# Optimization experiments

Measured on AMD Instinct MI355X. Metric: run time of the kernel, lower is better.

The kernel has to match this reference:

```python
import jax, jax.numpy as jnp
import numpy as np

N_NODES = 40000
N_EDGES = 640000
IN_CH = 128
OUT_CH = 128
BN_EPS = 1e-5


def setup_inputs() -> dict:
    key = jax.random.key(0)
    ks = jax.random.split(key, 8)
    x = jax.random.normal(ks[0], (N_NODES, IN_CH), dtype=jnp.float32)
    edge_index = jax.random.randint(ks[1], (2, N_EDGES), 0, N_NODES, dtype=jnp.int64)
    s1 = 1.0 / np.sqrt(IN_CH)
    s2 = 1.0 / np.sqrt(OUT_CH)
    W1 = jax.random.uniform(ks[2], (OUT_CH, IN_CH), jnp.float32, -s1, s1)
    b1 = jax.random.uniform(ks[3], (OUT_CH,), jnp.float32, -s1, s1)
    gamma = jnp.ones((OUT_CH,), jnp.float32)
    beta = jnp.zeros((OUT_CH,), jnp.float32)
    W2 = jax.random.uniform(ks[4], (OUT_CH, OUT_CH), jnp.float32, -s2, s2)
    b2 = jax.random.uniform(ks[5], (OUT_CH,), jnp.float32, -s2, s2)
    eps = jnp.float32(0.0)
    return {"x": x, "edge_index": edge_index, "W1": W1, "b1": b1,
            "gamma": gamma, "beta": beta, "W2": W2, "b2": b2, "eps": eps}


def reference(x, edge_index, W1, b1, gamma, beta, W2, b2, eps):
    src, dst = edge_index[0], edge_index[1]
    # neighbor sum: agg[v] = sum_{(u,v) in E} x[u]
    agg = jax.ops.segment_sum(x[src], dst, num_segments=N_NODES)  # [N, in_ch]
    h = (1.0 + eps) * x + agg
    # Linear 1
    h = h @ W1.T + b1  # [N, out_ch]
    # BatchNorm1d (training mode: batch stats, biased variance)
    mu = jnp.mean(h, axis=0)
    var = jnp.var(h, axis=0)
    h = (h - mu) * jax.lax.rsqrt(var + BN_EPS) * gamma + beta
    # ReLU + Linear 2
    h = jnp.maximum(h, 0.0)
    return h @ W2.T + b2
```

## Files before the change

### kernel.cpp

```cpp
#include <hip/hip_runtime.h>

#define NN 40000
#define NE 640000
#define BN_EPS 1e-5f

typedef __attribute__((ext_vector_type(8))) short bf16x8;
typedef __attribute__((ext_vector_type(4))) float f32x4;
typedef unsigned int uint;
typedef unsigned short ushort;

__device__ __forceinline__ float blo(uint u) { return __uint_as_float(u << 16); }
__device__ __forceinline__ float bhi(uint u) { return __uint_as_float(u & 0xFFFF0000u); }
__device__ __forceinline__ uint bpack(float lo, float hi) {
    uint a = __float_as_uint(lo); a = (a + 0x7FFFu + ((a >> 16) & 1u)) >> 16;
    uint b = __float_as_uint(hi); b = (b + 0x7FFFu + ((b >> 16) & 1u)) & 0xFFFF0000u;
    return a | b;
}
__device__ __forceinline__ ushort b1pack(float v) {
    uint u = __float_as_uint(v); return (ushort)((u + 0x7FFFu + ((u >> 16) & 1u)) >> 16);
}
__device__ __forceinline__ uint4 cvt8(const float4* f4, int i) {
    float4 p = f4[i * 2], q = f4[i * 2 + 1];
    uint4 o;
    o.x = bpack(p.x, p.y); o.y = bpack(p.z, p.w);
    o.z = bpack(q.x, q.y); o.w = bpack(q.z, q.w);
    return o;
}

__global__ __launch_bounds__(256) void k_pre(const float* __restrict__ x, const float* __restrict__ W1,
                                             const float* __restrict__ W2,
                                             int* __restrict__ cnt, float* __restrict__ bn,
                                             uint* __restrict__ xb, uint* __restrict__ w1b,
                                             uint* __restrict__ w2b) {
    int b = blockIdx.x, t = threadIdx.x;
    if (b < 157) {
        int i = b * 256 + t;
        if (i < NN) cnt[i] = 0;
        if (b == 156) bn[t] = 0.f;
    } else if (b < 2657) {
        int i = (b - 157) * 256 + t;
        ((uint4*)xb)[i] = cvt8((const float4*)x, i);
    } else if (b < 2665) {
        int i = (b - 2657) * 256 + t;
        ((uint4*)w1b)[i] = cvt8((const float4*)W1, i);
    } else {
        int i = (b - 2665) * 256 + t;
        ((uint4*)w2b)[i] = cvt8((const float4*)W2, i);
    }
}

__global__ __launch_bounds__(256) void k_bucket(const int* __restrict__ ei, int* __restrict__ cnt,
                                                ushort* __restrict__ srcl) {
    int e = blockIdx.x * 256 + threadIdx.x;
    if (e >= NE) return;
    int s = ei[e];
    int d = ei[NE + e];
    int pos = atomicAdd(&cnt[d], 1);
    if (pos < 64) srcl[d * 64 + pos] = (ushort)s;
}

__global__ __launch_bounds__(256) void k_gather(const uint* __restrict__ xbv, const int* __restrict__ cnt,
                                                const ushort* __restrict__ srcl, const float* __restrict__ epsp,
                                                uint* __restrict__ hb) {
    int wid = blockIdx.x * 4 + (threadIdx.x >> 6);
    int lane = threadIdx.x & 63;
    int deg = cnt[wid]; deg = deg > 64 ? 64 : deg;
    int sv = srcl[wid * 64 + lane];
    uint su = xbv[wid * 64 + lane];
    float e1 = 1.f + epsp[0];
    float a0 = blo(su) * e1, a1 = bhi(su) * e1;
    float c0 = 0.f, c1 = 0.f;
    int full = deg & ~7;
    for (int i = 0; i < full; i += 8) {
        int s0 = __builtin_amdgcn_readlane(sv, i);
        int s1 = __builtin_amdgcn_readlane(sv, i + 1);
        int s2 = __builtin_amdgcn_readlane(sv, i + 2);
        int s3 = __builtin_amdgcn_readlane(sv, i + 3);
        int s4 = __builtin_amdgcn_readlane(sv, i + 4);
        int s5 = __builtin_amdgcn_readlane(sv, i + 5);
        int s6 = __builtin_amdgcn_readlane(sv, i + 6);
        int s7 = __builtin_amdgcn_readlane(sv, i + 7);
        uint v0 = xbv[(size_t)s0 * 64 + lane];
        uint v1 = xbv[(size_t)s1 * 64 + lane];
        uint v2 = xbv[(size_t)s2 * 64 + lane];
        uint v3 = xbv[(size_t)s3 * 64 + lane];
        uint v4 = xbv[(size_t)s4 * 64 + lane];
        uint v5 = xbv[(size_t)s5 * 64 + lane];
        uint v6 = xbv[(size_t)s6 * 64 + lane];
        uint v7 = xbv[(size_t)s7 * 64 + lane];
        a0 += blo(v0) + blo(v1) + blo(v2) + blo(v3);
        c0 += blo(v4) + blo(v5) + blo(v6) + blo(v7);
        a1 += bhi(v0) + bhi(v1) + bhi(v2) + bhi(v3);
        c1 += bhi(v4) + bhi(v5) + bhi(v6) + bhi(v7);
    }
    if (deg & 7) {
#pragma unroll
        for (int j = 0; j < 8; ++j) {
            int idx = full + j;
            int s = __builtin_amdgcn_readlane(sv, idx);
            bool ok = idx < deg;
            s = ok ? s : 0;
            uint v = xbv[(size_t)s * 64 + lane];
            a0 += ok ? blo(v) : 0.f;
            a1 += ok ? bhi(v) : 0.f;
        }
    }
    hb[wid * 64 + lane] = bpack(a0 + c0, a1 + c1);
}

__global__ __launch_bounds__(256) void k_mm1(const ushort* __restrict__ hb, const ushort* __restrict__ w1b,
                                             const float* __restrict__ b1, ushort* __restrict__ h1b,
                                             float* __restrict__ bnsum, float* __restrict__ bnsumsq) {
    __shared__ float rs[256 * 8];
    __shared__ float rq[256 * 8];
    const int tid = threadIdx.x;
    const int wave = tid >> 6;
    const int lane = tid & 63;
    const int lr = lane & 15;
    const int lk = lane >> 4;
    const int r0 = (blockIdx.x * 4 + wave) * 16;

    bf16x8 a[4];
#pragma unroll
    for (int ks = 0; ks < 4; ++ks)
        a[ks] = *reinterpret_cast<const bf16x8*>(&hb[(size_t)(r0 + lr) * 128 + ks * 32 + lk * 8]);

    f32x4 acc[8];
#pragma unroll
    for (int t = 0; t < 8; ++t) { acc[t][0] = 0.f; acc[t][1] = 0.f; acc[t][2] = 0.f; acc[t][3] = 0.f; }

#pragma unroll
    for (int t = 0; t < 8; ++t) {
        const ushort* wrow = &w1b[(size_t)(t * 16 + lr) * 128];
#pragma unroll
        for (int ks = 0; ks < 4; ++ks) {
            bf16x8 bfr = *reinterpret_cast<const bf16x8*>(&wrow[ks * 32 + lk * 8]);
            acc[t] = __builtin_amdgcn_mfma_f32_16x16x32_bf16(a[ks], bfr, acc[t], 0, 0, 0);
        }
    }
#pragma unroll
    for (int t = 0; t < 8; ++t) {
        float bias = b1[t * 16 + lr];
        float s = 0.f, q = 0.f;
#pragma unroll
        for (int i = 0; i < 4; ++i) {
            float v = acc[t][i] + bias;
            h1b[(size_t)(r0 + lk * 4 + i) * 128 + t * 16 + lr] = b1pack(v);
            s += v; q += v * v;
        }
        rs[tid * 8 + t] = s;
        rq[tid * 8 + t] = q;
    }
    __syncthreads();
    if (tid < 128) {
        int c = tid, t = c >> 4, cr = c & 15;
        float s = 0.f, q = 0.f;
#pragma unroll
        for (int w = 0; w < 4; ++w)
#pragma unroll
            for (int g = 0; g < 4; ++g) {
                int src = w * 64 + g * 16 + cr;
                s += rs[src * 8 + t];
                q += rq[src * 8 + t];
            }
        atomicAdd(&bnsum[c], s);
        atomicAdd(&bnsumsq[c], q);
    }
}

__global__ __launch_bounds__(256) void k_mm2(const ushort* __restrict__ h1b, const ushort* __restrict__ w2b,
                                             const float* __restrict__ b2,
                                             const float* __restrict__ bnsum, const float* __restrict__ bnsumsq,
                                             const float* __restrict__ gamma, const float* __restrict__ beta,
                                             float* __restrict__ out) {
    __shared__ float ssc[128], ssh[128];
    const int tid = threadIdx.x;
    if (tid < 128) {
        float mu = bnsum[tid] * (1.0f / NN);
        float var = bnsumsq[tid] * (1.0f / NN) - mu * mu;
        float rsv = rsqrtf(var + BN_EPS);
        float g = rsv * gamma[tid];
        ssc[tid] = g;
        ssh[tid] = beta[tid] - mu * g;
    }
    __syncthreads();

    const int wave = tid >> 6;
    const int lane = tid & 63;
    const int lr = lane & 15;
    const int lk = lane >> 4;
    const int r0 = (blockIdx.x * 4 + wave) * 16;

    bf16x8 a[4];
#pragma unroll
    for (int ks = 0; ks < 4; ++ks) {
        int kbase = ks * 32 + lk * 8;
        bf16x8 raw = *reinterpret_cast<const bf16x8*>(&h1b[(size_t)(r0 + lr) * 128 + kbase]);
        bf16x8 o;
#pragma unroll
        for (int j = 0; j < 8; ++j) {
            float v = __uint_as_float(((uint)(ushort)raw[j]) << 16);
            v = fmaxf(0.f, fmaf(v, ssc[kbase + j], ssh[kbase + j]));
            o[j] = (short)b1pack(v);
        }
        a[ks] = o;
    }

    f32x4 acc[8];
#pragma unroll
    for (int t = 0; t < 8; ++t) { acc[t][0] = 0.f; acc[t][1] = 0.f; acc[t][2] = 0.f; acc[t][3] = 0.f; }

#pragma unroll
    for (int t = 0; t < 8; ++t) {
        const ushort* wrow = &w2b[(size_t)(t * 16 + lr) * 128];
#pragma unroll
        for (int ks = 0; ks < 4; ++ks) {
            bf16x8 bfr = *reinterpret_cast<const bf16x8*>(&wrow[ks * 32 + lk * 8]);
            acc[t] = __builtin_amdgcn_mfma_f32_16x16x32_bf16(a[ks], bfr, acc[t], 0, 0, 0);
        }
    }
#pragma unroll
    for (int t = 0; t < 8; ++t) {
        float bias = b2[t * 16 + lr];
#pragma unroll
        for (int i = 0; i < 4; ++i)
            out[(size_t)(r0 + lk * 4 + i) * 128 + t * 16 + lr] = acc[t][i] + bias;
    }
}

extern "C" void kernel_launch(void* const* d_in, const int* in_sizes, int n_in,
                              void* d_out, int out_size, void* d_ws, size_t ws_size,
                              hipStream_t stream) {
    const float* x     = (const float*)d_in[0];
    const int*   ei    = (const int*)d_in[1];
    const float* W1    = (const float*)d_in[2];
    const float* b1    = (const float*)d_in[3];
    const float* gamma = (const float*)d_in[4];
    const float* beta  = (const float*)d_in[5];
    const float* W2    = (const float*)d_in[6];
    const float* b2    = (const float*)d_in[7];
    const float* eps   = (const float*)d_in[8];

    char* ws = (char*)d_ws;
    int*    cnt  = (int*)(ws + 0);
    ushort* srcl = (ushort*)(ws + 196608);
    uint*   xb   = (uint*)(ws + 5373952);
    uint*   hb   = (uint*)(ws + 15728640);
    ushort* h1b  = (ushort*)(ws + 26083328);
    uint*   w1b  = (uint*)(ws + 36438016);
    uint*   w2b  = (uint*)(ws + 36503552);
    float*  bn   = (float*)(ws + 36569088);
    float* bnsum   = bn;
    float* bnsumsq = bn + 128;

    k_pre<<<2673, 256, 0, stream>>>(x, W1, W2, cnt, bn, xb, w1b, w2b);
    k_bucket<<<2500, 256, 0, stream>>>(ei, cnt, srcl);
    k_gather<<<10000, 256, 0, stream>>>(xb, cnt, srcl, eps, hb);
    k_mm1<<<625, 256, 0, stream>>>((const ushort*)hb, (const ushort*)w1b, b1, h1b, bnsum, bnsumsq);
    k_mm2<<<625, 256, 0, stream>>>(h1b, (const ushort*)w2b, b2, bnsum, bnsumsq, gamma, beta, (float*)d_out);
}
```

Baseline: 107.7 us.

## Gather neighbor rows with 16-byte loads, four neighbors per wave step

The gather kernel now splits each wave into four 16-lane groups. Each lane loads a uint4 holding 8 bf16 channels, so one wave instruction fetches four neighbor rows at once instead of one 4-byte word per lane per neighbor. Partial sums are combined across groups with xor shuffles, and a single group applies the self term and writes the result. The aim is fewer, wider memory instructions on a latency-bound random gather, at the cost of masked tail loads and the cross-lane reduction.

```diff
diff --git a/kernel.cpp b/kernel.cpp
--- a/kernel.cpp
+++ b/kernel.cpp
@@ -59,53 +59,56 @@
     if (pos < 64) srcl[d * 64 + pos] = (ushort)s;
 }
 
-__global__ __launch_bounds__(256) void k_gather(const uint* __restrict__ xbv, const int* __restrict__ cnt,
+__global__ __launch_bounds__(256) void k_gather(const uint4* __restrict__ xq, const int* __restrict__ cnt,
                                                 const ushort* __restrict__ srcl, const float* __restrict__ epsp,
-                                                uint* __restrict__ hb) {
+                                                uint4* __restrict__ hbq) {
     int wid = blockIdx.x * 4 + (threadIdx.x >> 6);
     int lane = threadIdx.x & 63;
+    int grp = lane >> 4;
+    int cidx = lane & 15;
     int deg = cnt[wid]; deg = deg > 64 ? 64 : deg;
     int sv = srcl[wid * 64 + lane];
-    uint su = xbv[wid * 64 + lane];
-    float e1 = 1.f + epsp[0];
-    float a0 = blo(su) * e1, a1 = bhi(su) * e1;
-    float c0 = 0.f, c1 = 0.f;
-    int full = deg & ~7;
-    for (int i = 0; i < full; i += 8) {
-        int s0 = __builtin_amdgcn_readlane(sv, i);
-        int s1 = __builtin_amdgcn_readlane(sv, i + 1);
-        int s2 = __builtin_amdgcn_readlane(sv, i + 2);
-        int s3 = __builtin_amdgcn_readlane(sv, i + 3);
-        int s4 = __builtin_amdgcn_readlane(sv, i + 4);
-        int s5 = __builtin_amdgcn_readlane(sv, i + 5);
-        int s6 = __builtin_amdgcn_readlane(sv, i + 6);
-        int s7 = __builtin_amdgcn_readlane(sv, i + 7);
-        uint v0 = xbv[(size_t)s0 * 64 + lane];
-        uint v1 = xbv[(size_t)s1 * 64 + lane];
-        uint v2 = xbv[(size_t)s2 * 64 + lane];
-        uint v3 = xbv[(size_t)s3 * 64 + lane];
-        uint v4 = xbv[(size_t)s4 * 64 + lane];
-        uint v5 = xbv[(size_t)s5 * 64 + lane];
-        uint v6 = xbv[(size_t)s6 * 64 + lane];
-        uint v7 = xbv[(size_t)s7 * 64 + lane];
-        a0 += blo(v0) + blo(v1) + blo(v2) + blo(v3);
-        c0 += blo(v4) + blo(v5) + blo(v6) + blo(v7);
-        a1 += bhi(v0) + bhi(v1) + bhi(v2) + bhi(v3);
-        c1 += bhi(v4) + bhi(v5) + bhi(v6) + bhi(v7);
-    }
-    if (deg & 7) {
-#pragma unroll
-        for (int j = 0; j < 8; ++j) {
-            int idx = full + j;
-            int s = __builtin_amdgcn_readlane(sv, idx);
-            bool ok = idx < deg;
-            s = ok ? s : 0;
-            uint v = xbv[(size_t)s * 64 + lane];
-            a0 += ok ? blo(v) : 0.f;
-            a1 += ok ? bhi(v) : 0.f;
-        }
-    }
-    hb[wid * 64 + lane] = bpack(a0 + c0, a1 + c1);
+
+    float acc[8];
+#pragma unroll
+    for (int j = 0; j < 8; ++j) acc[j] = 0.f;
+
+    int chunks = (deg + 7) >> 3;
+    for (int c = 0; c < chunks; ++c) {
+        int i = c * 8;
+        int n0 = i + grp, n1 = i + 4 + grp;
+        int s0 = __shfl(sv, n0);
+        int s1 = __shfl(sv, n1);
+        float m0 = n0 < deg ? 1.f : 0.f;
+        float m1 = n1 < deg ? 1.f : 0.f;
+        s0 = n0 < deg ? s0 : 0;
+        s1 = n1 < deg ? s1 : 0;
+        uint4 v0 = xq[(size_t)s0 * 16 + cidx];
+        uint4 v1 = xq[(size_t)s1 * 16 + cidx];
+        acc[0] = fmaf(blo(v0.x), m0, acc[0]); acc[1] = fmaf(bhi(v0.x), m0, acc[1]);
+        acc[2] = fmaf(blo(v0.y), m0, acc[2]); acc[3] = fmaf(bhi(v0.y), m0, acc[3]);
+        acc[4] = fmaf(blo(v0.z), m0, acc[4]); acc[5] = fmaf(bhi(v0.z), m0, acc[5]);
+        acc[6] = fmaf(blo(v0.w), m0, acc[6]); acc[7] = fmaf(bhi(v0.w), m0, acc[7]);
+        acc[0] = fmaf(blo(v1.x), m1, acc[0]); acc[1] = fmaf(bhi(v1.x), m1, acc[1]);
+        acc[2] = fmaf(blo(v1.y), m1, acc[2]); acc[3] = fmaf(bhi(v1.y), m1, acc[3]);
+        acc[4] = fmaf(blo(v1.z), m1, acc[4]); acc[5] = fmaf(bhi(v1.z), m1, acc[5]);
+        acc[6] = fmaf(blo(v1.w), m1, acc[6]); acc[7] = fmaf(bhi(v1.w), m1, acc[7]);
+    }
+#pragma unroll
+    for (int j = 0; j < 8; ++j) {
+        acc[j] += __shfl_xor(acc[j], 16);
+        acc[j] += __shfl_xor(acc[j], 32);
+    }
+    if (grp == 0) {
+        float e1 = 1.f + epsp[0];
+        uint4 s = xq[(size_t)wid * 16 + cidx];
+        uint4 o;
+        o.x = bpack(fmaf(blo(s.x), e1, acc[0]), fmaf(bhi(s.x), e1, acc[1]));
+        o.y = bpack(fmaf(blo(s.y), e1, acc[2]), fmaf(bhi(s.y), e1, acc[3]));
+        o.z = bpack(fmaf(blo(s.z), e1, acc[4]), fmaf(bhi(s.z), e1, acc[5]));
+        o.w = bpack(fmaf(blo(s.w), e1, acc[6]), fmaf(bhi(s.w), e1, acc[7]));
+        hbq[(size_t)wid * 16 + cidx] = o;
+    }
 }
 
 __global__ __launch_bounds__(256) void k_mm1(const ushort* __restrict__ hb, const ushort* __restrict__ w1b,
@@ -255,7 +258,7 @@
 
     k_pre<<<2673, 256, 0, stream>>>(x, W1, W2, cnt, bn, xb, w1b, w2b);
     k_bucket<<<2500, 256, 0, stream>>>(ei, cnt, srcl);
-    k_gather<<<10000, 256, 0, stream>>>(xb, cnt, srcl, eps, hb);
+    k_gather<<<10000, 256, 0, stream>>>((const uint4*)xb, cnt, srcl, eps, (uint4*)hb);
     k_mm1<<<625, 256, 0, stream>>>((const ushort*)hb, (const ushort*)w1b, b1, h1b, bnsum, bnsumsq);
     k_mm2<<<625, 256, 0, stream>>>(h1b, (const ushort*)w2b, b2, bnsum, bnsumsq, gamma, beta, (float*)d_out);
 }
```

Result: no change. 108.7 us (+1.0%).

## Fuse neighbor gather into first GEMM and merge bucketing with conversion

Applied to the files above, without the earlier changes.

The neighbor aggregation now runs inside the first GEMM kernel. Each wave gathers 16 nodes, two at a time, and writes the bf16 aggregated rows to shared memory instead of a global buffer. The edge bucketing is merged into the conversion kernel, and the count zeroing moves to a memset, cutting two launches and a full write and read of the intermediate h buffer. The trade-off is that the gather now runs on only 625 blocks instead of 10000, which may reduce the number of memory loads in flight and the latency hiding of the random gather.

```diff
diff --git a/kernel.cpp b/kernel.cpp
--- a/kernel.cpp
+++ b/kernel.cpp
@@ -27,103 +27,91 @@
     return o;
 }
 
-__global__ __launch_bounds__(256) void k_pre(const float* __restrict__ x, const float* __restrict__ W1,
-                                             const float* __restrict__ W2,
-                                             int* __restrict__ cnt, float* __restrict__ bn,
-                                             uint* __restrict__ xb, uint* __restrict__ w1b,
-                                             uint* __restrict__ w2b) {
+__global__ __launch_bounds__(256) void k_prep(const float* __restrict__ x, const float* __restrict__ W1,
+                                              const float* __restrict__ W2, const int* __restrict__ ei,
+                                              int* __restrict__ cnt, float* __restrict__ bn,
+                                              uint* __restrict__ xb, uint* __restrict__ w1b,
+                                              uint* __restrict__ w2b, ushort* __restrict__ srcl) {
     int b = blockIdx.x, t = threadIdx.x;
-    if (b < 157) {
-        int i = b * 256 + t;
-        if (i < NN) cnt[i] = 0;
-        if (b == 156) bn[t] = 0.f;
-    } else if (b < 2657) {
-        int i = (b - 157) * 256 + t;
+    if (b < 2500) {
+        int e = b * 256 + t;
+        int s = ei[e];
+        int d = ei[NE + e];
+        int pos = atomicAdd(&cnt[d], 1);
+        if (pos < 64) srcl[d * 64 + pos] = (ushort)s;
+    } else if (b < 5000) {
+        int i = (b - 2500) * 256 + t;
         ((uint4*)xb)[i] = cvt8((const float4*)x, i);
-    } else if (b < 2665) {
-        int i = (b - 2657) * 256 + t;
+    } else if (b < 5008) {
+        int i = (b - 5000) * 256 + t;
         ((uint4*)w1b)[i] = cvt8((const float4*)W1, i);
+    } else if (b < 5016) {
+        int i = (b - 5008) * 256 + t;
+        ((uint4*)w2b)[i] = cvt8((const float4*)W2, i);
     } else {
-        int i = (b - 2665) * 256 + t;
-        ((uint4*)w2b)[i] = cvt8((const float4*)W2, i);
-    }
-}
-
-__global__ __launch_bounds__(256) void k_bucket(const int* __restrict__ ei, int* __restrict__ cnt,
-                                                ushort* __restrict__ srcl) {
-    int e = blockIdx.x * 256 + threadIdx.x;
-    if (e >= NE) return;
-    int s = ei[e];
-    int d = ei[NE + e];
-    int pos = atomicAdd(&cnt[d], 1);
-    if (pos < 64) srcl[d * 64 + pos] = (ushort)s;
-}
-
-__global__ __launch_bounds__(256) void k_gather(const uint* __restrict__ xbv, const int* __restrict__ cnt,
-                                                const ushort* __restrict__ srcl, const float* __restrict__ epsp,
-                                                uint* __restrict__ hb) {
-    int wid = blockIdx.x * 4 + (threadIdx.x >> 6);
-    int lane = threadIdx.x & 63;
-    int deg = cnt[wid]; deg = deg > 64 ? 64 : deg;
-    int sv = srcl[wid * 64 + lane];
-    uint su = xbv[wid * 64 + lane];
-    float e1 = 1.f + epsp[0];
-    float a0 = blo(su) * e1, a1 = bhi(su) * e1;
-    float c0 = 0.f, c1 = 0.f;
-    int full = deg & ~7;
-    for (int i = 0; i < full; i += 8) {
-        int s0 = __builtin_amdgcn_readlane(sv, i);
-        int s1 = __builtin_amdgcn_readlane(sv, i + 1);
-        int s2 = __builtin_amdgcn_readlane(sv, i + 2);
-        int s3 = __builtin_amdgcn_readlane(sv, i + 3);
-        int s4 = __builtin_amdgcn_readlane(sv, i + 4);
-        int s5 = __builtin_amdgcn_readlane(sv, i + 5);
-        int s6 = __builtin_amdgcn_readlane(sv, i + 6);
-        int s7 = __builtin_amdgcn_readlane(sv, i + 7);
-        uint v0 = xbv[(size_t)s0 * 64 + lane];
-        uint v1 = xbv[(size_t)s1 * 64 + lane];
-        uint v2 = xbv[(size_t)s2 * 64 + lane];
-        uint v3 = xbv[(size_t)s3 * 64 + lane];
-        uint v4 = xbv[(size_t)s4 * 64 + lane];
-        uint v5 = xbv[(size_t)s5 * 64 + lane];
-        uint v6 = xbv[(size_t)s6 * 64 + lane];
-        uint v7 = xbv[(size_t)s7 * 64 + lane];
-        a0 += blo(v0) + blo(v1) + blo(v2) + blo(v3);
-        c0 += blo(v4) + blo(v5) + blo(v6) + blo(v7);
-        a1 += bhi(v0) + bhi(v1) + bhi(v2) + bhi(v3);
-        c1 += bhi(v4) + bhi(v5) + bhi(v6) + bhi(v7);
-    }
-    if (deg & 7) {
-#pragma unroll
-        for (int j = 0; j < 8; ++j) {
-            int idx = full + j;
-            int s = __builtin_amdgcn_readlane(sv, idx);
-            bool ok = idx < deg;
-            s = ok ? s : 0;
-            uint v = xbv[(size_t)s * 64 + lane];
-            a0 += ok ? blo(v) : 0.f;
-            a1 += ok ? bhi(v) : 0.f;
-        }
-    }
-    hb[wid * 64 + lane] = bpack(a0 + c0, a1 + c1);
-}
-
-__global__ __launch_bounds__(256) void k_mm1(const ushort* __restrict__ hb, const ushort* __restrict__ w1b,
-                                             const float* __restrict__ b1, ushort* __restrict__ h1b,
-                                             float* __restrict__ bnsum, float* __restrict__ bnsumsq) {
-    __shared__ float rs[256 * 8];
-    __shared__ float rq[256 * 8];
+        bn[t] = 0.f;
+    }
+}
+
+__device__ __forceinline__ void gchunk(int sv, int deg, int i, int lane,
+                                       const uint* __restrict__ xbv, float& a0, float& a1) {
+#pragma unroll
+    for (int j = 0; j < 8; ++j) {
+        int idx = i + j;
+        int s = __builtin_amdgcn_readlane(sv, idx);
+        bool ok = idx < deg;
+        s = ok ? s : 0;
+        uint v = xbv[(size_t)s * 64 + lane];
+        a0 += ok ? blo(v) : 0.f;
+        a1 += ok ? bhi(v) : 0.f;
+    }
+}
+
+__global__ __launch_bounds__(256) void k_gmm1(const uint* __restrict__ xbv, const int* __restrict__ cnt,
+                                              const ushort* __restrict__ srcl, const float* __restrict__ epsp,
+                                              const ushort* __restrict__ w1b, const float* __restrict__ b1,
+                                              ushort* __restrict__ h1b,
+                                              float* __restrict__ bnsum, float* __restrict__ bnsumsq) {
+    __shared__ alignas(16) char smem[17408];
+    uint* hu = (uint*)smem;
     const int tid = threadIdx.x;
     const int wave = tid >> 6;
     const int lane = tid & 63;
+    const float e1 = 1.f + epsp[0];
+    const int nbase = blockIdx.x * 64 + wave * 16;
+
+    for (int p = 0; p < 8; ++p) {
+        int nA = nbase + p * 2, nB = nA + 1;
+        int degA = cnt[nA]; degA = degA > 64 ? 64 : degA;
+        int degB = cnt[nB]; degB = degB > 64 ? 64 : degB;
+        int svA = srcl[(size_t)nA * 64 + lane];
+        int svB = srcl[(size_t)nB * 64 + lane];
+        uint suA = xbv[(size_t)nA * 64 + lane];
+        uint suB = xbv[(size_t)nB * 64 + lane];
+        float a0A = blo(suA) * e1, a1A = bhi(suA) * e1;
+        float a0B = blo(suB) * e1, a1B = bhi(suB) * e1;
+        int cA = (degA + 7) >> 3, cB = (degB + 7) >> 3;
+        int cm = cA > cB ? cA : cB;
+        for (int c = 0; c < cm; ++c) {
+            gchunk(svA, degA, c * 8, lane, xbv, a0A, a1A);
+            gchunk(svB, degB, c * 8, lane, xbv, a0B, a1B);
+        }
+        int rA = wave * 16 + p * 2;
+        hu[rA * 68 + lane]       = bpack(a0A, a1A);
+        hu[(rA + 1) * 68 + lane] = bpack(a0B, a1B);
+    }
+    __syncthreads();
+
     const int lr = lane & 15;
     const int lk = lane >> 4;
-    const int r0 = (blockIdx.x * 4 + wave) * 16;
+    const int r0l = wave * 16;
+    const int r0 = blockIdx.x * 64 + r0l;
 
     bf16x8 a[4];
 #pragma unroll
     for (int ks = 0; ks < 4; ++ks)
-        a[ks] = *reinterpret_cast<const bf16x8*>(&hb[(size_t)(r0 + lr) * 128 + ks * 32 + lk * 8]);
+        a[ks] = *reinterpret_cast<const bf16x8*>((const ushort*)smem + (r0l + lr) * 136 + ks * 32 + lk * 8);
+    __syncthreads();
 
     f32x4 acc[8];
 #pragma unroll
@@ -138,6 +126,9 @@
             acc[t] = __builtin_amdgcn_mfma_f32_16x16x32_bf16(a[ks], bfr, acc[t], 0, 0, 0);
         }
     }
+
+    float* rs = (float*)smem;
+    float* rq = rs + 2048;
 #pragma unroll
     for (int t = 0; t < 8; ++t) {
         float bias = b1[t * 16 + lr];
@@ -243,19 +234,17 @@
 
     char* ws = (char*)d_ws;
     int*    cnt  = (int*)(ws + 0);
-    ushort* srcl = (ushort*)(ws + 196608);
-    uint*   xb   = (uint*)(ws + 5373952);
-    uint*   hb   = (uint*)(ws + 15728640);
-    ushort* h1b  = (ushort*)(ws + 26083328);
-    uint*   w1b  = (uint*)(ws + 36438016);
-    uint*   w2b  = (uint*)(ws + 36503552);
-    float*  bn   = (float*)(ws + 36569088);
+    ushort* srcl = (ushort*)(ws + 160000);
+    uint*   xb   = (uint*)(ws + 5280000);
+    ushort* h1b  = (ushort*)(ws + 15520000);
+    uint*   w1b  = (uint*)(ws + 25760000);
+    uint*   w2b  = (uint*)(ws + 25792768);
+    float*  bn   = (float*)(ws + 25825536);
     float* bnsum   = bn;
     float* bnsumsq = bn + 128;
 
-    k_pre<<<2673, 256, 0, stream>>>(x, W1, W2, cnt, bn, xb, w1b, w2b);
-    k_bucket<<<2500, 256, 0, stream>>>(ei, cnt, srcl);
-    k_gather<<<10000, 256, 0, stream>>>(xb, cnt, srcl, eps, hb);
-    k_mm1<<<625, 256, 0, stream>>>((const ushort*)hb, (const ushort*)w1b, b1, h1b, bnsum, bnsumsq);
+    hipMemsetAsync(cnt, 0, 160000, stream);
+    k_prep<<<5017, 256, 0, stream>>>(x, W1, W2, ei, cnt, bn, xb, w1b, w2b, srcl);
+    k_gmm1<<<625, 256, 0, stream>>>(xb, cnt, srcl, eps, (const ushort*)w1b, b1, h1b, bnsum, bnsumsq);
     k_mm2<<<625, 256, 0, stream>>>(h1b, (const ushort*)w2b, b2, bnsum, bnsumsq, gamma, beta, (float*)d_out);
 }
```

After: 167.3 us. 55.4% more time.
